# Kernel optimization log

Hardware: AMD Instinct MI355X
Metric: run time of the kernel (lower is better)

## Reference

```python
import jax, jax.numpy as jnp
from jax import lax
import numpy as np

BATCH, SEQ, VOCAB, EMB, UNIT = 256, 512, 50000, 128, 512


def setup_inputs() -> dict:
    key = jax.random.key(0)
    ks = jax.random.split(key, 8)
    s = 0.05  # keep tanh out of saturation
    return {
        "tokens": jax.random.randint(ks[0], (BATCH, SEQ), 0, VOCAB, dtype=jnp.int32),
        "emb": jax.random.normal(ks[1], (VOCAB, EMB), jnp.float32) * s,
        "Wx0": jax.random.normal(ks[2], (EMB, UNIT), jnp.float32) * s,
        "Wh0": jax.random.normal(ks[3], (UNIT, UNIT), jnp.float32) * s,
        "b0": jnp.zeros((UNIT,), jnp.float32),
        "Wx1": jax.random.normal(ks[4], (UNIT, UNIT), jnp.float32) * s,
        "Wh1": jax.random.normal(ks[5], (UNIT, UNIT), jnp.float32) * s,
        "b1": jnp.zeros((UNIT,), jnp.float32),
        "fc_w": jax.random.normal(ks[6], (UNIT, 1), jnp.float32) * s,
        "fc_b": jnp.zeros((1,), jnp.float32),
    }


def reference(tokens, emb, Wx0, Wh0, b0, Wx1, Wh1, b1, fc_w, fc_b):
    # Embedding lookup: [B, T, E]
    x = emb[tokens]
    B = tokens.shape[0]
    U = Wh0.shape[0]

    def step(carry, xt):
        h0, h1, h2 = carry
        # SimpleRNNCell: h' = tanh(x @ Wx + h @ Wh + b); dropout inactive (training=None)
        h0n = jnp.tanh(xt @ Wx0 + h0 @ Wh0 + b0)
        # NOTE: original code reuses rnncell1 weights for both layer 1 and layer 2 (bug kept)
        h1n = jnp.tanh(h0n @ Wx1 + h1 @ Wh1 + b1)
        h2n = jnp.tanh(h1n @ Wx1 + h2 @ Wh1 + b1)
        return (h0n, h1n, h2n), None

    init = tuple(jnp.zeros((B, U), x.dtype) for _ in range(3))
    (h0, h1, h2), _ = lax.scan(step, init, jnp.swapaxes(x, 0, 1))  # scan over time [T, B, E]
    logits = h2 @ fc_w + fc_b  # [B, 1]
    return jax.nn.sigmoid(logits)
```

## Files before the change

### kernel.cpp

```cpp
#include <hip/hip_runtime.h>


#define BATCH 256
#define SEQ   512
#define EMBD  128
#define UNIT  512

typedef _Float16 half8 __attribute__((ext_vector_type(8)));
typedef _Float16 half4 __attribute__((ext_vector_type(4)));
typedef float    f32x4 __attribute__((ext_vector_type(4)));
typedef unsigned int uint4v __attribute__((ext_vector_type(4)));
typedef int      int4v __attribute__((ext_vector_type(4)));

#define FLAGS_BYTES 4096
#define HBUF_OFF    4096
#define HBUF_ELEMS  (3*8*4*32*512)
#define HBUF_BYTES  (HBUF_ELEMS*2)
#define PWX0_OFF    (HBUF_OFF + HBUF_BYTES)
#define PWH0_OFF    (PWX0_OFF + EMBD*UNIT*2)
#define PWX1_OFF    (PWH0_OFF + UNIT*UNIT*2)
#define PWH1_OFF    (PWX1_OFF + UNIT*UNIT*2)

__device__ __forceinline__ void sc_st_int(int* p, int v) {
    asm volatile("global_store_dword %0, %1, off sc0 sc1" :: "v"(p), "v"(v) : "memory");
}

__device__ __forceinline__ void sc_ld_q3(const int* p0, const int* p1, const int* p2,
                                         int4v& a, int4v& b, int4v& c) {
    asm volatile(
        "global_load_dwordx4 %0, %3, off sc0 sc1\n\t"
        "global_load_dwordx4 %1, %4, off sc0 sc1\n\t"
        "global_load_dwordx4 %2, %5, off sc0 sc1\n\t"
        "s_waitcnt vmcnt(0)"
        : "=&v"(a), "=&v"(b), "=&v"(c)
        : "v"(p0), "v"(p1), "v"(p2)
        : "memory");
}

__device__ __forceinline__ void sc_load14(
    const uint4v* a0, const uint4v* a1, const uint4v* a2,
    const uint4v* a3, const uint4v* a4, const uint4v* a5,
    const uint4v* b0, const uint4v* b1, const uint4v* b2, const uint4v* b3,
    const uint4v* b4, const uint4v* b5, const uint4v* b6, const uint4v* b7,
    uint4v& s0, uint4v& s1, uint4v& s2, uint4v& s3, uint4v& s4, uint4v& s5,
    uint4v& r0, uint4v& r1, uint4v& r2, uint4v& r3,
    uint4v& r4, uint4v& r5, uint4v& r6, uint4v& r7)
{
    asm volatile(
        "global_load_dwordx4 %0, %14, off sc0 sc1\n\t"
        "global_load_dwordx4 %1, %15, off sc0 sc1\n\t"
        "global_load_dwordx4 %2, %16, off sc0 sc1\n\t"
        "global_load_dwordx4 %3, %17, off sc0 sc1\n\t"
        "global_load_dwordx4 %4, %18, off sc0 sc1\n\t"
        "global_load_dwordx4 %5, %19, off sc0 sc1\n\t"
        "global_load_dwordx4 %6, %20, off sc0 sc1\n\t"
        "global_load_dwordx4 %7, %21, off sc0 sc1\n\t"
        "global_load_dwordx4 %8, %22, off sc0 sc1\n\t"
        "global_load_dwordx4 %9, %23, off sc0 sc1\n\t"
        "global_load_dwordx4 %10, %24, off sc0 sc1\n\t"
        "global_load_dwordx4 %11, %25, off sc0 sc1\n\t"
        "global_load_dwordx4 %12, %26, off sc0 sc1\n\t"
        "global_load_dwordx4 %13, %27, off sc0 sc1\n\t"
        "s_waitcnt vmcnt(0)"
        : "=&v"(s0), "=&v"(s1), "=&v"(s2), "=&v"(s3), "=&v"(s4), "=&v"(s5),
          "=&v"(r0), "=&v"(r1), "=&v"(r2), "=&v"(r3),
          "=&v"(r4), "=&v"(r5), "=&v"(r6), "=&v"(r7)
        : "v"(a0), "v"(a1), "v"(a2), "v"(a3), "v"(a4), "v"(a5),
          "v"(b0), "v"(b1), "v"(b2), "v"(b3), "v"(b4), "v"(b5), "v"(b6), "v"(b7)
        : "memory");
}

__device__ __forceinline__ void sc_load6(
    const uint4v* p0, const uint4v* p1, const uint4v* p2,
    const uint4v* p3, const uint4v* p4, const uint4v* p5,
    uint4v& r0, uint4v& r1, uint4v& r2, uint4v& r3, uint4v& r4, uint4v& r5)
{
    asm volatile(
        "global_load_dwordx4 %0, %6, off sc0 sc1\n\t"
        "global_load_dwordx4 %1, %7, off sc0 sc1\n\t"
        "global_load_dwordx4 %2, %8, off sc0 sc1\n\t"
        "global_load_dwordx4 %3, %9, off sc0 sc1\n\t"
        "global_load_dwordx4 %4, %10, off sc0 sc1\n\t"
        "global_load_dwordx4 %5, %11, off sc0 sc1\n\t"
        "s_waitcnt vmcnt(0)"
        : "=&v"(r0), "=&v"(r1), "=&v"(r2), "=&v"(r3), "=&v"(r4), "=&v"(r5)
        : "v"(p0), "v"(p1), "v"(p2), "v"(p3), "v"(p4), "v"(p5)
        : "memory");
}

__device__ __forceinline__ void sc_store2(uint4v* p0, uint4v v0, uint4v* p1, uint4v v1) {
    asm volatile(
        "global_store_dwordx4 %0, %2, off sc0 sc1\n\t"
        "global_store_dwordx4 %1, %3, off sc0 sc1\n\t"
        "s_waitcnt vmcnt(0)"
        :: "v"(p0), "v"(p1), "v"(v0), "v"(v1)
        : "memory");
}

__global__ void zero_ws_kernel(uint4v* __restrict__ p, int n16) {
    int i = blockIdx.x * 256 + threadIdx.x;
    uint4v z = {0u, 0u, 0u, 0u};
    if (i < n16) p[i] = z;
}

__global__ void pack_w_kernel(const float* __restrict__ src, _Float16* __restrict__ dst,
                              int K, int N) {
    int idx = blockIdx.x * 256 + threadIdx.x;
    if (idx >= K * N) return;
    int j    = idx & 7;
    int lane = (idx >> 3) & 63;
    int rest = idx >> 9;
    int KT   = K >> 5;
    int kt   = rest % KT;
    int nt   = rest / KT;
    int k = kt*32 + (lane >> 4)*8 + j;
    int n = nt*16 + (lane & 15);
    dst[idx] = (_Float16)src[k * N + n];
}

__global__ __launch_bounds__(256, 1)
void rnn_main_kernel(const int*   __restrict__ tokens,
                     const float* __restrict__ emb,
                     const float* __restrict__ b0,
                     const float* __restrict__ b1,
                     char* ws)
{
    const int bid   = blockIdx.x;
    const int layer = bid >> 5;
    const int mg    = (bid >> 2) & 7;
    const int ns    = bid & 3;
    const int tid   = threadIdx.x;
    const int wv    = tid >> 6;
    const int lane  = tid & 63;
    const int q     = lane >> 4;
    const int c16   = lane & 15;

    int* flags = (int*)ws;
    int* qOwn  = flags + (layer*8 + mg)*32;
    int* qUp   = flags + ((layer > 0 ? layer-1 : layer)*8 + mg)*32;
    int* qDn   = flags + ((layer < 2 ? layer+1 : layer)*8 + mg)*32;

    _Float16* hbuf = (_Float16*)(ws + HBUF_OFF);
    const _Float16* pWh = (const _Float16*)(ws + (layer == 0 ? PWH0_OFF : PWH1_OFF));
    const _Float16* pWx = (const _Float16*)(ws + (layer == 0 ? PWX0_OFF : PWX1_OFF));
    const float* bias = (layer == 0) ? b0 : b1;

    const int c0  = ns*128 + wv*32;
    const int nt0 = c0 >> 4;

    __shared__ _Float16 Ah [32][512];
    __shared__ _Float16 Ain[32][512];
    __shared__ _Float16 Bounce[32][128];

    {
        uint4v z = {0u,0u,0u,0u};
#pragma unroll
        for (int i = 0; i < 8; ++i) ((uint4v*)Ah)[i*256 + tid] = z;
    }

    half8 whf[16][2];
    half8 wxf[16][2];
#pragma unroll
    for (int kt = 0; kt < 16; ++kt)
#pragma unroll
        for (int n = 0; n < 2; ++n)
            whf[kt][n] = *(const half8*)&pWh[(((nt0 + n)*16 + kt)*64 + lane) * 8];
    if (layer == 0) {
#pragma unroll
        for (int kt = 0; kt < 4; ++kt)
#pragma unroll
            for (int n = 0; n < 2; ++n)
                wxf[kt][n] = *(const half8*)&pWx[(((nt0 + n)*4 + kt)*64 + lane) * 8];
    } else {
#pragma unroll
        for (int kt = 0; kt < 16; ++kt)
#pragma unroll
            for (int n = 0; n < 2; ++n)
                wxf[kt][n] = *(const half8*)&pWx[(((nt0 + n)*16 + kt)*64 + lane) * 8];
    }

    const float bv0 = bias[c0 + c16];
    const float bv1 = bias[c0 + 16 + c16];

    const int m0       = mg * 32;
    const int slotBase = (layer*8 + mg) * 4;

    const int sA = (ns == 0) ? 1 : 0;
    const int sB = (ns <= 1) ? 2 : 1;
    const int sC = (ns <= 2) ? 3 : 2;

    for (int t = 0; t < SEQ; ++t) {
        if (tid == 0) {
            for (;;) {
                int4v o, u, d;
                sc_ld_q3(qOwn, qUp, qDn, o, u, d);
                int mo = o[0] < o[1] ? o[0] : o[1];
                mo = mo < o[2] ? mo : o[2]; mo = mo < o[3] ? mo : o[3];
                int mu = u[0] < u[1] ? u[0] : u[1];
                mu = mu < u[2] ? mu : u[2]; mu = mu < u[3] ? mu : u[3];
                int md = d[0] < d[1] ? d[0] : d[1];
                md = md < d[2] ? md : d[2]; md = md < d[3] ? md : d[3];
                bool ok = (mo >= t);
                if (layer > 0)            ok = ok && (mu >= t + 1);
                if (layer < 2 && t >= 4)  ok = ok && (md >= t - 3);
                if (ok) break;
                __builtin_amdgcn_s_sleep(1);
            }
        }
        __syncthreads();

        const uint4v* tp = (const uint4v*)(hbuf + (slotBase + ((t + 3) & 3)) * 16384);
        const int j0 = 2*tid, j1 = j0 + 1;
        const int r0i = j0 >> 4, cl0 = j0 & 15;
        const int r1i = j1 >> 4, cl1 = j1 & 15;
        const int ccA0 = sA*16 + cl0, ccA1 = sA*16 + cl1;
        const int ccB0 = sB*16 + cl0, ccB1 = sB*16 + cl1;
        const int ccC0 = sC*16 + cl0, ccC1 = sC*16 + cl1;

        f32x4 acc00 = {0,0,0,0}, acc01 = {0,0,0,0}, acc10 = {0,0,0,0}, acc11 = {0,0,0,0};

        if (layer > 0) {
            const uint4v* sb = (const uint4v*)
                (hbuf + (((layer-1)*8 + mg)*4 + (t & 3)) * 16384);
            uint4v s0,s1,s2,s3,s4,s5, rr0,rr1,rr2,rr3,rr4,rr5,rr6,rr7;
            sc_load14(tp + r0i*64 + ccA0, tp + r1i*64 + ccA1,
                      tp + r0i*64 + ccB0, tp + r1i*64 + ccB1,
                      tp + r0i*64 + ccC0, tp + r1i*64 + ccC1,
                      sb +        tid, sb +  256 + tid, sb +  512 + tid, sb +  768 + tid,
                      sb + 1024 + tid, sb + 1280 + tid, sb + 1536 + tid, sb + 1792 + tid,
                      s0, s1, s2, s3, s4, s5,
                      rr0, rr1, rr2, rr3, rr4, rr5, rr6, rr7);
            *(uint4v*)&Ah[r0i][((ccA0 + r0i) & 63) * 8] = s0;
            *(uint4v*)&Ah[r1i][((ccA1 + r1i) & 63) * 8] = s1;
            *(uint4v*)&Ah[r0i][((ccB0 + r0i) & 63) * 8] = s2;
            *(uint4v*)&Ah[r1i][((ccB1 + r1i) & 63) * 8] = s3;
            *(uint4v*)&Ah[r0i][((ccC0 + r0i) & 63) * 8] = s4;
            *(uint4v*)&Ah[r1i][((ccC1 + r1i) & 63) * 8] = s5;
#pragma unroll
            for (int i = 0; i < 8; ++i) {
                uint4v v = (i==0)?rr0:(i==1)?rr1:(i==2)?rr2:(i==3)?rr3:
                           (i==4)?rr4:(i==5)?rr5:(i==6)?rr6:rr7;
                int ci = i*256 + tid;
                int r  = ci >> 6;
                int cc = ci & 63;
                *(uint4v*)&Ain[r][((cc + r) & 63) * 8] = v;
            }
            __syncthreads();

#pragma unroll
            for (int kt = 0; kt < 16; ++kt) {
                half8 a0 = *(const half8*)&Ah[c16]     [((kt*4 + q + c16)      & 63) * 8];
                half8 a1 = *(const half8*)&Ah[16 + c16][((kt*4 + q + 16 + c16) & 63) * 8];
                acc00 = __builtin_amdgcn_mfma_f32_16x16x32_f16(a0, whf[kt][0], acc00, 0, 0, 0);
                acc01 = __builtin_amdgcn_mfma_f32_16x16x32_f16(a0, whf[kt][1], acc01, 0, 0, 0);
                acc10 = __builtin_amdgcn_mfma_f32_16x16x32_f16(a1, whf[kt][0], acc10, 0, 0, 0);
                acc11 = __builtin_amdgcn_mfma_f32_16x16x32_f16(a1, whf[kt][1], acc11, 0, 0, 0);
            }
#pragma unroll
            for (int kt = 0; kt < 16; ++kt) {
                half8 a0 = *(const half8*)&Ain[c16]     [((kt*4 + q + c16)      & 63) * 8];
                half8 a1 = *(const half8*)&Ain[16 + c16][((kt*4 + q + 16 + c16) & 63) * 8];
                acc00 = __builtin_amdgcn_mfma_f32_16x16x32_f16(a0, wxf[kt][0], acc00, 0, 0, 0);
                acc01 = __builtin_amdgcn_mfma_f32_16x16x32_f16(a0, wxf[kt][1], acc01, 0, 0, 0);
                acc10 = __builtin_amdgcn_mfma_f32_16x16x32_f16(a1, wxf[kt][0], acc10, 0, 0, 0);
                acc11 = __builtin_amdgcn_mfma_f32_16x16x32_f16(a1, wxf[kt][1], acc11, 0, 0, 0);
            }
        } else {
            uint4v s0, s1, s2, s3, s4, s5;
            sc_load6(tp + r0i*64 + ccA0, tp + r1i*64 + ccA1,
                     tp + r0i*64 + ccB0, tp + r1i*64 + ccB1,
                     tp + r0i*64 + ccC0, tp + r1i*64 + ccC1,
                     s0, s1, s2, s3, s4, s5);
            *(uint4v*)&Ah[r0i][((ccA0 + r0i) & 63) * 8] = s0;
            *(uint4v*)&Ah[r1i][((ccA1 + r1i) & 63) * 8] = s1;
            *(uint4v*)&Ah[r0i][((ccB0 + r0i) & 63) * 8] = s2;
            *(uint4v*)&Ah[r1i][((ccB1 + r1i) & 63) * 8] = s3;
            *(uint4v*)&Ah[r0i][((ccC0 + r0i) & 63) * 8] = s4;
            *(uint4v*)&Ah[r1i][((ccC1 + r1i) & 63) * 8] = s5;
#pragma unroll
            for (int i = 0; i < 4; ++i) {
                int idx = i*256 + tid;
                int r   = idx >> 5;
                int qq  = idx & 31;
                int tok = tokens[(m0 + r)*SEQ + t];
                float4 f = *((const float4*)(emb + (long)tok * EMBD) + qq);
                half4 h = { (_Float16)f.x, (_Float16)f.y, (_Float16)f.z, (_Float16)f.w };
                *(half4*)&Ain[r][((((qq >> 1) + r) & 63) * 8) + (qq & 1) * 4] = h;
            }
            __syncthreads();

#pragma unroll
            for (int kt = 0; kt < 16; ++kt) {
                half8 a0 = *(const half8*)&Ah[c16]     [((kt*4 + q + c16)      & 63) * 8];
                half8 a1 = *(const half8*)&Ah[16 + c16][((kt*4 + q + 16 + c16) & 63) * 8];
                acc00 = __builtin_amdgcn_mfma_f32_16x16x32_f16(a0, whf[kt][0], acc00, 0, 0, 0);
                acc01 = __builtin_amdgcn_mfma_f32_16x16x32_f16(a0, whf[kt][1], acc01, 0, 0, 0);
                acc10 = __builtin_amdgcn_mfma_f32_16x16x32_f16(a1, whf[kt][0], acc10, 0, 0, 0);
                acc11 = __builtin_amdgcn_mfma_f32_16x16x32_f16(a1, whf[kt][1], acc11, 0, 0, 0);
            }
#pragma unroll
            for (int kt = 0; kt < 4; ++kt) {
                half8 a0 = *(const half8*)&Ain[c16]     [((kt*4 + q + c16)      & 63) * 8];
                half8 a1 = *(const half8*)&Ain[16 + c16][((kt*4 + q + 16 + c16) & 63) * 8];
                acc00 = __builtin_amdgcn_mfma_f32_16x16x32_f16(a0, wxf[kt][0], acc00, 0, 0, 0);
                acc01 = __builtin_amdgcn_mfma_f32_16x16x32_f16(a0, wxf[kt][1], acc01, 0, 0, 0);
                acc10 = __builtin_amdgcn_mfma_f32_16x16x32_f16(a1, wxf[kt][0], acc10, 0, 0, 0);
                acc11 = __builtin_amdgcn_mfma_f32_16x16x32_f16(a1, wxf[kt][1], acc11, 0, 0, 0);
            }
        }

        _Float16 hv[16];
#pragma unroll
        for (int r = 0; r < 4; ++r) {
            int row0 = q*4 + r, row1 = 16 + row0;
            float z, e; _Float16 v;
            z = acc00[r] + bv0; e = __expf(2.0f*z); v = (_Float16)(1.0f - 2.0f/(e + 1.0f));
            hv[r*4+0] = v; Bounce[row0][wv*32 + c16]      = v;
            z = acc01[r] + bv1; e = __expf(2.0f*z); v = (_Float16)(1.0f - 2.0f/(e + 1.0f));
            hv[r*4+1] = v; Bounce[row0][wv*32 + 16 + c16] = v;
            z = acc10[r] + bv0; e = __expf(2.0f*z); v = (_Float16)(1.0f - 2.0f/(e + 1.0f));
            hv[r*4+2] = v; Bounce[row1][wv*32 + c16]      = v;
            z = acc11[r] + bv1; e = __expf(2.0f*z); v = (_Float16)(1.0f - 2.0f/(e + 1.0f));
            hv[r*4+3] = v; Bounce[row1][wv*32 + 16 + c16] = v;
        }
        __syncthreads();

        {
            int g0 = c0 + c16, g1 = c0 + 16 + c16;
#pragma unroll
            for (int r = 0; r < 4; ++r) {
                int row0 = q*4 + r, row1 = 16 + row0;
                Ah[row0][(((g0 >> 3) + row0) & 63)*8 + (g0 & 7)] = hv[r*4+0];
                Ah[row0][(((g1 >> 3) + row0) & 63)*8 + (g1 & 7)] = hv[r*4+1];
                Ah[row1][(((g0 >> 3) + row1) & 63)*8 + (g0 & 7)] = hv[r*4+2];
                Ah[row1][(((g1 >> 3) + row1) & 63)*8 + (g1 & 7)] = hv[r*4+3];
            }
            _Float16* tc = hbuf + (slotBase + (t & 3)) * 16384;
            uint4v v0 = ((const uint4v*)Bounce)[j0];
            uint4v v1 = ((const uint4v*)Bounce)[j1];
            uint4v* d0 = (uint4v*)(tc + (j0 >> 4)*512 + ns*128) + (j0 & 15);
            uint4v* d1 = (uint4v*)(tc + (j1 >> 4)*512 + ns*128) + (j1 & 15);
            sc_store2(d0, v0, d1, v1);
        }
        __syncthreads();
        if (tid == 0) sc_st_int(qOwn + ns, t + 1);
    }
}

__global__ void fc_kernel(const char* __restrict__ ws,
                          const float* __restrict__ fc_w,
                          const float* __restrict__ fc_b,
                          float* __restrict__ out)
{
    int row  = blockIdx.x;
    int lane = threadIdx.x;
    int m = row >> 5, lr = row & 31;
    const _Float16* h2 = (const _Float16*)(ws + HBUF_OFF)
                         + (((2*8 + m)*4 + 3) * 16384)
                         + lr * UNIT;
    half8 hv = *(const half8*)&h2[lane * 8];
    const float* w = fc_w + lane * 8;
    float s = 0.0f;
#pragma unroll
    for (int j = 0; j < 8; ++j) s += (float)hv[j] * w[j];
#pragma unroll
    for (int off = 32; off > 0; off >>= 1) s += __shfl_down(s, off);
    if (lane == 0) {
        float logit = s + fc_b[0];
        out[row] = 1.0f / (1.0f + __expf(-logit));
    }
}

extern "C" void kernel_launch(void* const* d_in, const int* in_sizes, int n_in,
                              void* d_out, int out_size, void* d_ws, size_t ws_size,
                              hipStream_t stream)
{
    const int*   tokens = (const int*)  d_in[0];
    const float* emb    = (const float*)d_in[1];
    const float* Wx0    = (const float*)d_in[2];
    const float* Wh0    = (const float*)d_in[3];
    const float* b0     = (const float*)d_in[4];
    const float* Wx1    = (const float*)d_in[5];
    const float* Wh1    = (const float*)d_in[6];
    const float* b1     = (const float*)d_in[7];
    const float* fcw    = (const float*)d_in[8];
    const float* fcb    = (const float*)d_in[9];
    char*  ws  = (char*)d_ws;
    float* out = (float*)d_out;

    int n16 = (FLAGS_BYTES + HBUF_BYTES) / 16;
    zero_ws_kernel<<<(n16 + 255)/256, 256, 0, stream>>>((uint4v*)ws, n16);

    pack_w_kernel<<<(EMBD*UNIT + 255)/256, 256, 0, stream>>>(Wx0, (_Float16*)(ws + PWX0_OFF), EMBD, UNIT);
    pack_w_kernel<<<(UNIT*UNIT + 255)/256, 256, 0, stream>>>(Wh0, (_Float16*)(ws + PWH0_OFF), UNIT, UNIT);
    pack_w_kernel<<<(UNIT*UNIT + 255)/256, 256, 0, stream>>>(Wx1, (_Float16*)(ws + PWX1_OFF), UNIT, UNIT);
    pack_w_kernel<<<(UNIT*UNIT + 255)/256, 256, 0, stream>>>(Wh1, (_Float16*)(ws + PWH1_OFF), UNIT, UNIT);

    rnn_main_kernel<<<96, 256, 0, stream>>>(tokens, emb, b0, b1, ws);

    fc_kernel<<<256, 64, 0, stream>>>((const char*)ws, fcw, fcb, out);
}
```

Baseline: 2.632 ms.

## Piggyback flag reads on data loads to skip spin-wait and prefetch embeddings

The peer-progress flags are now loaded in the same batched coherent load as the hidden-state data. Their minimum is cached in shared memory, so the per-step spin-wait and its barrier can be skipped when earlier reads already show the dependencies are met. Layer 0 also prefetches the next step's embedding rows into registers during the current step and writes them to LDS after the MMA work. This hides the gather latency but adds registers and some extra flag loads.

```diff
diff --git a/kernel.cpp b/kernel.cpp
--- a/kernel.cpp
+++ b/kernel.cpp
@@ -23,6 +23,12 @@
 
 __device__ __forceinline__ void sc_st_int(int* p, int v) {
     asm volatile("global_store_dword %0, %1, off sc0 sc1" :: "v"(p), "v"(v) : "memory");
+}
+
+__device__ __forceinline__ int min4(int4v v) {
+    int a = v[0] < v[1] ? v[0] : v[1];
+    int b = v[2] < v[3] ? v[2] : v[3];
+    return a < b ? a : b;
 }
 
 __device__ __forceinline__ void sc_ld_q3(const int* p0, const int* p1, const int* p2,
@@ -37,54 +43,68 @@
         : "memory");
 }
 
-__device__ __forceinline__ void sc_load14(
+__device__ __forceinline__ void sc_load17(
     const uint4v* a0, const uint4v* a1, const uint4v* a2,
     const uint4v* a3, const uint4v* a4, const uint4v* a5,
     const uint4v* b0, const uint4v* b1, const uint4v* b2, const uint4v* b3,
     const uint4v* b4, const uint4v* b5, const uint4v* b6, const uint4v* b7,
+    const int* f0, const int* f1, const int* f2,
     uint4v& s0, uint4v& s1, uint4v& s2, uint4v& s3, uint4v& s4, uint4v& s5,
     uint4v& r0, uint4v& r1, uint4v& r2, uint4v& r3,
-    uint4v& r4, uint4v& r5, uint4v& r6, uint4v& r7)
+    uint4v& r4, uint4v& r5, uint4v& r6, uint4v& r7,
+    int4v& q0, int4v& q1, int4v& q2)
 {
     asm volatile(
-        "global_load_dwordx4 %0, %14, off sc0 sc1\n\t"
-        "global_load_dwordx4 %1, %15, off sc0 sc1\n\t"
-        "global_load_dwordx4 %2, %16, off sc0 sc1\n\t"
-        "global_load_dwordx4 %3, %17, off sc0 sc1\n\t"
-        "global_load_dwordx4 %4, %18, off sc0 sc1\n\t"
-        "global_load_dwordx4 %5, %19, off sc0 sc1\n\t"
-        "global_load_dwordx4 %6, %20, off sc0 sc1\n\t"
-        "global_load_dwordx4 %7, %21, off sc0 sc1\n\t"
-        "global_load_dwordx4 %8, %22, off sc0 sc1\n\t"
-        "global_load_dwordx4 %9, %23, off sc0 sc1\n\t"
-        "global_load_dwordx4 %10, %24, off sc0 sc1\n\t"
-        "global_load_dwordx4 %11, %25, off sc0 sc1\n\t"
-        "global_load_dwordx4 %12, %26, off sc0 sc1\n\t"
-        "global_load_dwordx4 %13, %27, off sc0 sc1\n\t"
+        "global_load_dwordx4 %0, %17, off sc0 sc1\n\t"
+        "global_load_dwordx4 %1, %18, off sc0 sc1\n\t"
+        "global_load_dwordx4 %2, %19, off sc0 sc1\n\t"
+        "global_load_dwordx4 %3, %20, off sc0 sc1\n\t"
+        "global_load_dwordx4 %4, %21, off sc0 sc1\n\t"
+        "global_load_dwordx4 %5, %22, off sc0 sc1\n\t"
+        "global_load_dwordx4 %6, %23, off sc0 sc1\n\t"
+        "global_load_dwordx4 %7, %24, off sc0 sc1\n\t"
+        "global_load_dwordx4 %8, %25, off sc0 sc1\n\t"
+        "global_load_dwordx4 %9, %26, off sc0 sc1\n\t"
+        "global_load_dwordx4 %10, %27, off sc0 sc1\n\t"
+        "global_load_dwordx4 %11, %28, off sc0 sc1\n\t"
+        "global_load_dwordx4 %12, %29, off sc0 sc1\n\t"
+        "global_load_dwordx4 %13, %30, off sc0 sc1\n\t"
+        "global_load_dwordx4 %14, %31, off sc0 sc1\n\t"
+        "global_load_dwordx4 %15, %32, off sc0 sc1\n\t"
+        "global_load_dwordx4 %16, %33, off sc0 sc1\n\t"
         "s_waitcnt vmcnt(0)"
         : "=&v"(s0), "=&v"(s1), "=&v"(s2), "=&v"(s3), "=&v"(s4), "=&v"(s5),
           "=&v"(r0), "=&v"(r1), "=&v"(r2), "=&v"(r3),
-          "=&v"(r4), "=&v"(r5), "=&v"(r6), "=&v"(r7)
+          "=&v"(r4), "=&v"(r5), "=&v"(r6), "=&v"(r7),
+          "=&v"(q0), "=&v"(q1), "=&v"(q2)
         : "v"(a0), "v"(a1), "v"(a2), "v"(a3), "v"(a4), "v"(a5),
-          "v"(b0), "v"(b1), "v"(b2), "v"(b3), "v"(b4), "v"(b5), "v"(b6), "v"(b7)
+          "v"(b0), "v"(b1), "v"(b2), "v"(b3), "v"(b4), "v"(b5), "v"(b6), "v"(b7),
+          "v"(f0), "v"(f1), "v"(f2)
         : "memory");
 }
 
-__device__ __forceinline__ void sc_load6(
+__device__ __forceinline__ void sc_load9(
     const uint4v* p0, const uint4v* p1, const uint4v* p2,
     const uint4v* p3, const uint4v* p4, const uint4v* p5,
-    uint4v& r0, uint4v& r1, uint4v& r2, uint4v& r3, uint4v& r4, uint4v& r5)
+    const int* f0, const int* f1, const int* f2,
+    uint4v& r0, uint4v& r1, uint4v& r2, uint4v& r3, uint4v& r4, uint4v& r5,
+    int4v& q0, int4v& q1, int4v& q2)
 {
     asm volatile(
-        "global_load_dwordx4 %0, %6, off sc0 sc1\n\t"
-        "global_load_dwordx4 %1, %7, off sc0 sc1\n\t"
-        "global_load_dwordx4 %2, %8, off sc0 sc1\n\t"
-        "global_load_dwordx4 %3, %9, off sc0 sc1\n\t"
-        "global_load_dwordx4 %4, %10, off sc0 sc1\n\t"
-        "global_load_dwordx4 %5, %11, off sc0 sc1\n\t"
+        "global_load_dwordx4 %0, %9, off sc0 sc1\n\t"
+        "global_load_dwordx4 %1, %10, off sc0 sc1\n\t"
+        "global_load_dwordx4 %2, %11, off sc0 sc1\n\t"
+        "global_load_dwordx4 %3, %12, off sc0 sc1\n\t"
+        "global_load_dwordx4 %4, %13, off sc0 sc1\n\t"
+        "global_load_dwordx4 %5, %14, off sc0 sc1\n\t"
+        "global_load_dwordx4 %6, %15, off sc0 sc1\n\t"
+        "global_load_dwordx4 %7, %16, off sc0 sc1\n\t"
+        "global_load_dwordx4 %8, %17, off sc0 sc1\n\t"
         "s_waitcnt vmcnt(0)"
-        : "=&v"(r0), "=&v"(r1), "=&v"(r2), "=&v"(r3), "=&v"(r4), "=&v"(r5)
-        : "v"(p0), "v"(p1), "v"(p2), "v"(p3), "v"(p4), "v"(p5)
+        : "=&v"(r0), "=&v"(r1), "=&v"(r2), "=&v"(r3), "=&v"(r4), "=&v"(r5),
+          "=&v"(q0), "=&v"(q1), "=&v"(q2)
+        : "v"(p0), "v"(p1), "v"(p2), "v"(p3), "v"(p4), "v"(p5),
+          "v"(f0), "v"(f1), "v"(f2)
         : "memory");
 }
 
@@ -151,12 +171,14 @@
     __shared__ _Float16 Ah [32][512];
     __shared__ _Float16 Ain[32][512];
     __shared__ _Float16 Bounce[32][128];
+    __shared__ int      SkipInfo[4];
 
     {
         uint4v z = {0u,0u,0u,0u};
 #pragma unroll
         for (int i = 0; i < 8; ++i) ((uint4v*)Ah)[i*256 + tid] = z;
     }
+    if (tid < 4) SkipInfo[tid] = -1000000;
 
     half8 whf[16][2];
     half8 wxf[16][2];
@@ -189,25 +211,42 @@
     const int sB = (ns <= 1) ? 2 : 1;
     const int sC = (ns <= 2) ? 3 : 2;
 
+    if (layer == 0) {
+#pragma unroll
+        for (int i = 0; i < 4; ++i) {
+            int idx = i*256 + tid;
+            int r   = idx >> 5;
+            int qq  = idx & 31;
+            int tok = tokens[(m0 + r)*SEQ + 0];
+            float4 f = *((const float4*)(emb + (long)tok * EMBD) + qq);
+            half4 h = { (_Float16)f.x, (_Float16)f.y, (_Float16)f.z, (_Float16)f.w };
+            *(half4*)&Ain[r][((((qq >> 1) + r) & 63) * 8) + (qq & 1) * 4] = h;
+        }
+    }
+    __syncthreads();
+
     for (int t = 0; t < SEQ; ++t) {
-        if (tid == 0) {
-            for (;;) {
-                int4v o, u, d;
-                sc_ld_q3(qOwn, qUp, qDn, o, u, d);
-                int mo = o[0] < o[1] ? o[0] : o[1];
-                mo = mo < o[2] ? mo : o[2]; mo = mo < o[3] ? mo : o[3];
-                int mu = u[0] < u[1] ? u[0] : u[1];
-                mu = mu < u[2] ? mu : u[2]; mu = mu < u[3] ? mu : u[3];
-                int md = d[0] < d[1] ? d[0] : d[1];
-                md = md < d[2] ? md : d[2]; md = md < d[3] ? md : d[3];
-                bool ok = (mo >= t);
-                if (layer > 0)            ok = ok && (mu >= t + 1);
-                if (layer < 2 && t >= 4)  ok = ok && (md >= t - 3);
-                if (ok) break;
-                __builtin_amdgcn_s_sleep(1);
+        {
+            int mo = SkipInfo[0], mu = SkipInfo[1], md = SkipInfo[2];
+            bool skip = (mo >= t);
+            if (layer > 0)           skip = skip && (mu >= t + 1);
+            if (layer < 2 && t >= 4) skip = skip && (md >= t - 3);
+            if (!skip) {
+                if (tid == 0) {
+                    for (;;) {
+                        int4v o, u, d;
+                        sc_ld_q3(qOwn, qUp, qDn, o, u, d);
+                        int o_ = min4(o), u_ = min4(u), d_ = min4(d);
+                        bool ok = (o_ >= t);
+                        if (layer > 0)            ok = ok && (u_ >= t + 1);
+                        if (layer < 2 && t >= 4)  ok = ok && (d_ >= t - 3);
+                        if (ok) { SkipInfo[0]=o_; SkipInfo[1]=u_; SkipInfo[2]=d_; break; }
+                        __builtin_amdgcn_s_sleep(2);
+                    }
+                }
+                __syncthreads();
             }
         }
-        __syncthreads();
 
         const uint4v* tp = (const uint4v*)(hbuf + (slotBase + ((t + 3) & 3)) * 16384);
         const int j0 = 2*tid, j1 = j0 + 1;
@@ -218,18 +257,22 @@
         const int ccC0 = sC*16 + cl0, ccC1 = sC*16 + cl1;
 
         f32x4 acc00 = {0,0,0,0}, acc01 = {0,0,0,0}, acc10 = {0,0,0,0}, acc11 = {0,0,0,0};
+        int4v fq0, fq1, fq2;
+        float4 pg0, pg1, pg2, pg3;
 
         if (layer > 0) {
             const uint4v* sb = (const uint4v*)
                 (hbuf + (((layer-1)*8 + mg)*4 + (t & 3)) * 16384);
             uint4v s0,s1,s2,s3,s4,s5, rr0,rr1,rr2,rr3,rr4,rr5,rr6,rr7;
-            sc_load14(tp + r0i*64 + ccA0, tp + r1i*64 + ccA1,
+            sc_load17(tp + r0i*64 + ccA0, tp + r1i*64 + ccA1,
                       tp + r0i*64 + ccB0, tp + r1i*64 + ccB1,
                       tp + r0i*64 + ccC0, tp + r1i*64 + ccC1,
                       sb +        tid, sb +  256 + tid, sb +  512 + tid, sb +  768 + tid,
                       sb + 1024 + tid, sb + 1280 + tid, sb + 1536 + tid, sb + 1792 + tid,
+                      qOwn, qUp, qDn,
                       s0, s1, s2, s3, s4, s5,
-                      rr0, rr1, rr2, rr3, rr4, rr5, rr6, rr7);
+                      rr0, rr1, rr2, rr3, rr4, rr5, rr6, rr7,
+                      fq0, fq1, fq2);
             *(uint4v*)&Ah[r0i][((ccA0 + r0i) & 63) * 8] = s0;
             *(uint4v*)&Ah[r1i][((ccA1 + r1i) & 63) * 8] = s1;
             *(uint4v*)&Ah[r0i][((ccB0 + r0i) & 63) * 8] = s2;
@@ -267,25 +310,32 @@
             }
         } else {
             uint4v s0, s1, s2, s3, s4, s5;
-            sc_load6(tp + r0i*64 + ccA0, tp + r1i*64 + ccA1,
+            sc_load9(tp + r0i*64 + ccA0, tp + r1i*64 + ccA1,
                      tp + r0i*64 + ccB0, tp + r1i*64 + ccB1,
                      tp + r0i*64 + ccC0, tp + r1i*64 + ccC1,
-                     s0, s1, s2, s3, s4, s5);
+                     qOwn, qUp, qDn,
+                     s0, s1, s2, s3, s4, s5, fq0, fq1, fq2);
             *(uint4v*)&Ah[r0i][((ccA0 + r0i) & 63) * 8] = s0;
             *(uint4v*)&Ah[r1i][((ccA1 + r1i) & 63) * 8] = s1;
             *(uint4v*)&Ah[r0i][((ccB0 + r0i) & 63) * 8] = s2;
             *(uint4v*)&Ah[r1i][((ccB1 + r1i) & 63) * 8] = s3;
             *(uint4v*)&Ah[r0i][((ccC0 + r0i) & 63) * 8] = s4;
             *(uint4v*)&Ah[r1i][((ccC1 + r1i) & 63) * 8] = s5;
-#pragma unroll
-            for (int i = 0; i < 4; ++i) {
-                int idx = i*256 + tid;
-                int r   = idx >> 5;
-                int qq  = idx & 31;
-                int tok = tokens[(m0 + r)*SEQ + t];
-                float4 f = *((const float4*)(emb + (long)tok * EMBD) + qq);
-                half4 h = { (_Float16)f.x, (_Float16)f.y, (_Float16)f.z, (_Float16)f.w };
-                *(half4*)&Ain[r][((((qq >> 1) + r) & 63) * 8) + (qq & 1) * 4] = h;
+
+            {
+                int tn = (t + 1 < SEQ) ? t + 1 : SEQ - 1;
+                int idx0 = tid,        r0g = idx0 >> 5, q0g = idx0 & 31;
+                int idx1 = 256 + tid,  r1g = idx1 >> 5, q1g = idx1 & 31;
+                int idx2 = 512 + tid,  r2g = idx2 >> 5, q2g = idx2 & 31;
+                int idx3 = 768 + tid,  r3g = idx3 >> 5, q3g = idx3 & 31;
+                int t0 = tokens[(m0 + r0g)*SEQ + tn];
+                int t1 = tokens[(m0 + r1g)*SEQ + tn];
+                int t2 = tokens[(m0 + r2g)*SEQ + tn];
+                int t3 = tokens[(m0 + r3g)*SEQ + tn];
+                pg0 = *((const float4*)(emb + (long)t0 * EMBD) + q0g);
+                pg1 = *((const float4*)(emb + (long)t1 * EMBD) + q1g);
+                pg2 = *((const float4*)(emb + (long)t2 * EMBD) + q2g);
+                pg3 = *((const float4*)(emb + (long)t3 * EMBD) + q3g);
             }
             __syncthreads();
 
@@ -334,6 +384,22 @@
                 Ah[row0][(((g1 >> 3) + row0) & 63)*8 + (g1 & 7)] = hv[r*4+1];
                 Ah[row1][(((g0 >> 3) + row1) & 63)*8 + (g0 & 7)] = hv[r*4+2];
                 Ah[row1][(((g1 >> 3) + row1) & 63)*8 + (g1 & 7)] = hv[r*4+3];
+            }
+            if (layer == 0 && t + 1 < SEQ) {
+#pragma unroll
+                for (int i = 0; i < 4; ++i) {
+                    float4 f = (i==0)?pg0:(i==1)?pg1:(i==2)?pg2:pg3;
+                    int idx = i*256 + tid;
+                    int r   = idx >> 5;
+                    int qq  = idx & 31;
+                    half4 h = { (_Float16)f.x, (_Float16)f.y, (_Float16)f.z, (_Float16)f.w };
+                    *(half4*)&Ain[r][((((qq >> 1) + r) & 63) * 8) + (qq & 1) * 4] = h;
+                }
+            }
+            if (tid == 0) {
+                SkipInfo[0] = min4(fq0);
+                SkipInfo[1] = min4(fq1);
+                SkipInfo[2] = min4(fq2);
             }
             _Float16* tc = hbuf + (slotBase + (t & 3)) * 16384;
             uint4v v0 = ((const uint4v*)Bounce)[j0];
```

New measurement: 2.755 ms. 4.7% more time.

## Overlap input loads with recurrent MFMA via LDS DMA, prefetch, and XOR swizzle

Applied to the files above, without the earlier changes.

Layers 1 and 2 now pull the previous layer's hidden state straight into LDS with global_load_lds DMA. That DMA runs while the Wh MFMA loop executes, so the Wx loop waits only on its own barrier. Layer 0 prefetches the next step's embedding rows into registers during the current step and writes them to LDS after the tanh. The LDS layout changes from a rotate swizzle to an XOR swizzle, and the global h buffer is stored in the same swizzled order so the copy needs no per-element reshuffle; fc_kernel is adjusted to match. The code also replaces __syncthreads with lighter waitcnt+barrier sequences and adds a per-block staggered startup sleep, at the cost of more complex memory ordering that depends on the asm waitcnt choices being correct.

```diff
diff --git a/kernel.cpp b/kernel.cpp
--- a/kernel.cpp
+++ b/kernel.cpp
@@ -34,39 +34,6 @@
         "s_waitcnt vmcnt(0)"
         : "=&v"(a), "=&v"(b), "=&v"(c)
         : "v"(p0), "v"(p1), "v"(p2)
-        : "memory");
-}
-
-__device__ __forceinline__ void sc_load14(
-    const uint4v* a0, const uint4v* a1, const uint4v* a2,
-    const uint4v* a3, const uint4v* a4, const uint4v* a5,
-    const uint4v* b0, const uint4v* b1, const uint4v* b2, const uint4v* b3,
-    const uint4v* b4, const uint4v* b5, const uint4v* b6, const uint4v* b7,
-    uint4v& s0, uint4v& s1, uint4v& s2, uint4v& s3, uint4v& s4, uint4v& s5,
-    uint4v& r0, uint4v& r1, uint4v& r2, uint4v& r3,
-    uint4v& r4, uint4v& r5, uint4v& r6, uint4v& r7)
-{
-    asm volatile(
-        "global_load_dwordx4 %0, %14, off sc0 sc1\n\t"
-        "global_load_dwordx4 %1, %15, off sc0 sc1\n\t"
-        "global_load_dwordx4 %2, %16, off sc0 sc1\n\t"
-        "global_load_dwordx4 %3, %17, off sc0 sc1\n\t"
-        "global_load_dwordx4 %4, %18, off sc0 sc1\n\t"
-        "global_load_dwordx4 %5, %19, off sc0 sc1\n\t"
-        "global_load_dwordx4 %6, %20, off sc0 sc1\n\t"
-        "global_load_dwordx4 %7, %21, off sc0 sc1\n\t"
-        "global_load_dwordx4 %8, %22, off sc0 sc1\n\t"
-        "global_load_dwordx4 %9, %23, off sc0 sc1\n\t"
-        "global_load_dwordx4 %10, %24, off sc0 sc1\n\t"
-        "global_load_dwordx4 %11, %25, off sc0 sc1\n\t"
-        "global_load_dwordx4 %12, %26, off sc0 sc1\n\t"
-        "global_load_dwordx4 %13, %27, off sc0 sc1\n\t"
-        "s_waitcnt vmcnt(0)"
-        : "=&v"(s0), "=&v"(s1), "=&v"(s2), "=&v"(s3), "=&v"(s4), "=&v"(s5),
-          "=&v"(r0), "=&v"(r1), "=&v"(r2), "=&v"(r3),
-          "=&v"(r4), "=&v"(r5), "=&v"(r6), "=&v"(r7)
-        : "v"(a0), "v"(a1), "v"(a2), "v"(a3), "v"(a4), "v"(a5),
-          "v"(b0), "v"(b1), "v"(b2), "v"(b3), "v"(b4), "v"(b5), "v"(b6), "v"(b7)
         : "memory");
 }
 
@@ -97,6 +64,23 @@
         : "memory");
 }
 
+__device__ __forceinline__ void bar_lgkm() {
+    asm volatile("s_waitcnt lgkmcnt(0)\n\ts_barrier" ::: "memory");
+}
+__device__ __forceinline__ void bar_vm_lgkm() {
+    asm volatile("s_waitcnt vmcnt(0) lgkmcnt(0)\n\ts_barrier" ::: "memory");
+}
+__device__ __forceinline__ void bar_only() {
+    asm volatile("s_barrier" ::: "memory");
+}
+
+__device__ __forceinline__ void lds_dma16(const void* g, void* l) {
+    __builtin_amdgcn_global_load_lds(
+        (const __attribute__((address_space(1))) void*)g,
+        (__attribute__((address_space(3))) void*)l,
+        16, 0, 17);
+}
+
 __global__ void zero_ws_kernel(uint4v* __restrict__ p, int n16) {
     int i = blockIdx.x * 256 + threadIdx.x;
     uint4v z = {0u, 0u, 0u, 0u};
@@ -134,6 +118,9 @@
     const int lane  = tid & 63;
     const int q     = lane >> 4;
     const int c16   = lane & 15;
+    const int xq    = c16 & 7;
+
+    for (int i = 0; i < mg; ++i) { __builtin_amdgcn_s_sleep(8); __builtin_amdgcn_s_sleep(8); }
 
     int* flags = (int*)ws;
     int* qOwn  = flags + (layer*8 + mg)*32;
@@ -188,6 +175,31 @@
     const int sA = (ns == 0) ? 1 : 0;
     const int sB = (ns <= 1) ? 2 : 1;
     const int sC = (ns <= 2) ? 3 : 2;
+
+    const int j0 = 2*tid, j1 = j0 + 1;
+    const int r0i = j0 >> 4, cl0 = j0 & 15;
+    const int r1i = j1 >> 4, cl1 = j1 & 15;
+    const int k0 = r0i & 7, k1 = r1i & 7;
+    const int pA0 = sA*16 + cl0, pA1 = sA*16 + cl1;
+    const int pB0 = sB*16 + cl0, pB1 = sB*16 + cl1;
+    const int pC0 = sC*16 + cl0, pC1 = sC*16 + cl1;
+    const int pO0 = (ns*16 + cl0) ^ k0;
+    const int pO1 = (ns*16 + cl1) ^ k1;
+
+    if (layer == 0) {
+#pragma unroll
+        for (int i = 0; i < 4; ++i) {
+            int idx = i*256 + tid;
+            int r   = idx >> 5;
+            int qq  = idx & 31;
+            int tok = tokens[(m0 + r)*SEQ + 0];
+            float4 f = *((const float4*)(emb + (long)tok * EMBD) + qq);
+            half4 h = { (_Float16)f.x, (_Float16)f.y, (_Float16)f.z, (_Float16)f.w };
+            int pc = (qq >> 1) ^ (r & 7);
+            *(half4*)&Ain[r][pc*8 + (qq & 1)*4] = h;
+        }
+    }
+    __syncthreads();
 
     for (int t = 0; t < SEQ; ++t) {
         if (tid == 0) {
@@ -207,101 +219,78 @@
                 __builtin_amdgcn_s_sleep(1);
             }
         }
-        __syncthreads();
+        bar_only();
 
         const uint4v* tp = (const uint4v*)(hbuf + (slotBase + ((t + 3) & 3)) * 16384);
-        const int j0 = 2*tid, j1 = j0 + 1;
-        const int r0i = j0 >> 4, cl0 = j0 & 15;
-        const int r1i = j1 >> 4, cl1 = j1 & 15;
-        const int ccA0 = sA*16 + cl0, ccA1 = sA*16 + cl1;
-        const int ccB0 = sB*16 + cl0, ccB1 = sB*16 + cl1;
-        const int ccC0 = sC*16 + cl0, ccC1 = sC*16 + cl1;
+
+        {
+            uint4v s0, s1, s2, s3, s4, s5;
+            sc_load6(tp + r0i*64 + pA0, tp + r1i*64 + pA1,
+                     tp + r0i*64 + pB0, tp + r1i*64 + pB1,
+                     tp + r0i*64 + pC0, tp + r1i*64 + pC1,
+                     s0, s1, s2, s3, s4, s5);
+            *(uint4v*)&Ah[r0i][pA0 * 8] = s0;
+            *(uint4v*)&Ah[r1i][pA1 * 8] = s1;
+            *(uint4v*)&Ah[r0i][pB0 * 8] = s2;
+            *(uint4v*)&Ah[r1i][pB1 * 8] = s3;
+            *(uint4v*)&Ah[r0i][pC0 * 8] = s4;
+            *(uint4v*)&Ah[r1i][pC1 * 8] = s5;
+        }
+
+        float4 pg0, pg1, pg2, pg3;
+        if (layer > 0) {
+            const _Float16* sb = hbuf + (((layer-1)*8 + mg)*4 + (t & 3)) * 16384;
+#pragma unroll
+            for (int i = 0; i < 8; ++i) {
+                int row = wv*8 + i;
+                lds_dma16(sb + row*512 + lane*8, &Ain[row][0]);
+            }
+        } else {
+            int tn = (t + 1 < SEQ) ? t + 1 : SEQ - 1;
+            int idx0 = tid,        r0g = idx0 >> 5, q0g = idx0 & 31;
+            int idx1 = 256 + tid,  r1g = idx1 >> 5, q1g = idx1 & 31;
+            int idx2 = 512 + tid,  r2g = idx2 >> 5, q2g = idx2 & 31;
+            int idx3 = 768 + tid,  r3g = idx3 >> 5, q3g = idx3 & 31;
+            int t0 = tokens[(m0 + r0g)*SEQ + tn];
+            int t1 = tokens[(m0 + r1g)*SEQ + tn];
+            int t2 = tokens[(m0 + r2g)*SEQ + tn];
+            int t3 = tokens[(m0 + r3g)*SEQ + tn];
+            pg0 = *((const float4*)(emb + (long)t0 * EMBD) + q0g);
+            pg1 = *((const float4*)(emb + (long)t1 * EMBD) + q1g);
+            pg2 = *((const float4*)(emb + (long)t2 * EMBD) + q2g);
+            pg3 = *((const float4*)(emb + (long)t3 * EMBD) + q3g);
+        }
+
+        bar_lgkm();
 
         f32x4 acc00 = {0,0,0,0}, acc01 = {0,0,0,0}, acc10 = {0,0,0,0}, acc11 = {0,0,0,0};
 
+#pragma unroll
+        for (int kt = 0; kt < 16; ++kt) {
+            half8 a0 = *(const half8*)&Ah[c16]     [((kt*4 + q) ^ xq) * 8];
+            half8 a1 = *(const half8*)&Ah[16 + c16][((kt*4 + q) ^ xq) * 8];
+            acc00 = __builtin_amdgcn_mfma_f32_16x16x32_f16(a0, whf[kt][0], acc00, 0, 0, 0);
+            acc01 = __builtin_amdgcn_mfma_f32_16x16x32_f16(a0, whf[kt][1], acc01, 0, 0, 0);
+            acc10 = __builtin_amdgcn_mfma_f32_16x16x32_f16(a1, whf[kt][0], acc10, 0, 0, 0);
+            acc11 = __builtin_amdgcn_mfma_f32_16x16x32_f16(a1, whf[kt][1], acc11, 0, 0, 0);
+        }
+
         if (layer > 0) {
-            const uint4v* sb = (const uint4v*)
-                (hbuf + (((layer-1)*8 + mg)*4 + (t & 3)) * 16384);
-            uint4v s0,s1,s2,s3,s4,s5, rr0,rr1,rr2,rr3,rr4,rr5,rr6,rr7;
-            sc_load14(tp + r0i*64 + ccA0, tp + r1i*64 + ccA1,
-                      tp + r0i*64 + ccB0, tp + r1i*64 + ccB1,
-                      tp + r0i*64 + ccC0, tp + r1i*64 + ccC1,
-                      sb +        tid, sb +  256 + tid, sb +  512 + tid, sb +  768 + tid,
-                      sb + 1024 + tid, sb + 1280 + tid, sb + 1536 + tid, sb + 1792 + tid,
-                      s0, s1, s2, s3, s4, s5,
-                      rr0, rr1, rr2, rr3, rr4, rr5, rr6, rr7);
-            *(uint4v*)&Ah[r0i][((ccA0 + r0i) & 63) * 8] = s0;
-            *(uint4v*)&Ah[r1i][((ccA1 + r1i) & 63) * 8] = s1;
-            *(uint4v*)&Ah[r0i][((ccB0 + r0i) & 63) * 8] = s2;
-            *(uint4v*)&Ah[r1i][((ccB1 + r1i) & 63) * 8] = s3;
-            *(uint4v*)&Ah[r0i][((ccC0 + r0i) & 63) * 8] = s4;
-            *(uint4v*)&Ah[r1i][((ccC1 + r1i) & 63) * 8] = s5;
-#pragma unroll
-            for (int i = 0; i < 8; ++i) {
-                uint4v v = (i==0)?rr0:(i==1)?rr1:(i==2)?rr2:(i==3)?rr3:
-                           (i==4)?rr4:(i==5)?rr5:(i==6)?rr6:rr7;
-                int ci = i*256 + tid;
-                int r  = ci >> 6;
-                int cc = ci & 63;
-                *(uint4v*)&Ain[r][((cc + r) & 63) * 8] = v;
-            }
-            __syncthreads();
-
+            bar_vm_lgkm();
 #pragma unroll
             for (int kt = 0; kt < 16; ++kt) {
-                half8 a0 = *(const half8*)&Ah[c16]     [((kt*4 + q + c16)      & 63) * 8];
-                half8 a1 = *(const half8*)&Ah[16 + c16][((kt*4 + q + 16 + c16) & 63) * 8];
-                acc00 = __builtin_amdgcn_mfma_f32_16x16x32_f16(a0, whf[kt][0], acc00, 0, 0, 0);
-                acc01 = __builtin_amdgcn_mfma_f32_16x16x32_f16(a0, whf[kt][1], acc01, 0, 0, 0);
-                acc10 = __builtin_amdgcn_mfma_f32_16x16x32_f16(a1, whf[kt][0], acc10, 0, 0, 0);
-                acc11 = __builtin_amdgcn_mfma_f32_16x16x32_f16(a1, whf[kt][1], acc11, 0, 0, 0);
-            }
-#pragma unroll
-            for (int kt = 0; kt < 16; ++kt) {
-                half8 a0 = *(const half8*)&Ain[c16]     [((kt*4 + q + c16)      & 63) * 8];
-                half8 a1 = *(const half8*)&Ain[16 + c16][((kt*4 + q + 16 + c16) & 63) * 8];
+                half8 a0 = *(const half8*)&Ain[c16]     [((kt*4 + q) ^ xq) * 8];
+                half8 a1 = *(const half8*)&Ain[16 + c16][((kt*4 + q) ^ xq) * 8];
                 acc00 = __builtin_amdgcn_mfma_f32_16x16x32_f16(a0, wxf[kt][0], acc00, 0, 0, 0);
                 acc01 = __builtin_amdgcn_mfma_f32_16x16x32_f16(a0, wxf[kt][1], acc01, 0, 0, 0);
                 acc10 = __builtin_amdgcn_mfma_f32_16x16x32_f16(a1, wxf[kt][0], acc10, 0, 0, 0);
                 acc11 = __builtin_amdgcn_mfma_f32_16x16x32_f16(a1, wxf[kt][1], acc11, 0, 0, 0);
             }
         } else {
-            uint4v s0, s1, s2, s3, s4, s5;
-            sc_load6(tp + r0i*64 + ccA0, tp + r1i*64 + ccA1,
-                     tp + r0i*64 + ccB0, tp + r1i*64 + ccB1,
-                     tp + r0i*64 + ccC0, tp + r1i*64 + ccC1,
-                     s0, s1, s2, s3, s4, s5);
-            *(uint4v*)&Ah[r0i][((ccA0 + r0i) & 63) * 8] = s0;
-            *(uint4v*)&Ah[r1i][((ccA1 + r1i) & 63) * 8] = s1;
-            *(uint4v*)&Ah[r0i][((ccB0 + r0i) & 63) * 8] = s2;
-            *(uint4v*)&Ah[r1i][((ccB1 + r1i) & 63) * 8] = s3;
-            *(uint4v*)&Ah[r0i][((ccC0 + r0i) & 63) * 8] = s4;
-            *(uint4v*)&Ah[r1i][((ccC1 + r1i) & 63) * 8] = s5;
-#pragma unroll
-            for (int i = 0; i < 4; ++i) {
-                int idx = i*256 + tid;
-                int r   = idx >> 5;
-                int qq  = idx & 31;
-                int tok = tokens[(m0 + r)*SEQ + t];
-                float4 f = *((const float4*)(emb + (long)tok * EMBD) + qq);
-                half4 h = { (_Float16)f.x, (_Float16)f.y, (_Float16)f.z, (_Float16)f.w };
-                *(half4*)&Ain[r][((((qq >> 1) + r) & 63) * 8) + (qq & 1) * 4] = h;
-            }
-            __syncthreads();
-
-#pragma unroll
-            for (int kt = 0; kt < 16; ++kt) {
-                half8 a0 = *(const half8*)&Ah[c16]     [((kt*4 + q + c16)      & 63) * 8];
-                half8 a1 = *(const half8*)&Ah[16 + c16][((kt*4 + q + 16 + c16) & 63) * 8];
-                acc00 = __builtin_amdgcn_mfma_f32_16x16x32_f16(a0, whf[kt][0], acc00, 0, 0, 0);
-                acc01 = __builtin_amdgcn_mfma_f32_16x16x32_f16(a0, whf[kt][1], acc01, 0, 0, 0);
-                acc10 = __builtin_amdgcn_mfma_f32_16x16x32_f16(a1, whf[kt][0], acc10, 0, 0, 0);
-                acc11 = __builtin_amdgcn_mfma_f32_16x16x32_f16(a1, whf[kt][1], acc11, 0, 0, 0);
-            }
 #pragma unroll
             for (int kt = 0; kt < 4; ++kt) {
-                half8 a0 = *(const half8*)&Ain[c16]     [((kt*4 + q + c16)      & 63) * 8];
-                half8 a1 = *(const half8*)&Ain[16 + c16][((kt*4 + q + 16 + c16) & 63) * 8];
+                half8 a0 = *(const half8*)&Ain[c16]     [((kt*4 + q) ^ xq) * 8];
+                half8 a1 = *(const half8*)&Ain[16 + c16][((kt*4 + q) ^ xq) * 8];
                 acc00 = __builtin_amdgcn_mfma_f32_16x16x32_f16(a0, wxf[kt][0], acc00, 0, 0, 0);
                 acc01 = __builtin_amdgcn_mfma_f32_16x16x32_f16(a0, wxf[kt][1], acc01, 0, 0, 0);
                 acc10 = __builtin_amdgcn_mfma_f32_16x16x32_f16(a1, wxf[kt][0], acc10, 0, 0, 0);
@@ -309,40 +298,43 @@
             }
         }
 
-        _Float16 hv[16];
 #pragma unroll
         for (int r = 0; r < 4; ++r) {
             int row0 = q*4 + r, row1 = 16 + row0;
-            float z, e; _Float16 v;
-            z = acc00[r] + bv0; e = __expf(2.0f*z); v = (_Float16)(1.0f - 2.0f/(e + 1.0f));
-            hv[r*4+0] = v; Bounce[row0][wv*32 + c16]      = v;
-            z = acc01[r] + bv1; e = __expf(2.0f*z); v = (_Float16)(1.0f - 2.0f/(e + 1.0f));
-            hv[r*4+1] = v; Bounce[row0][wv*32 + 16 + c16] = v;
-            z = acc10[r] + bv0; e = __expf(2.0f*z); v = (_Float16)(1.0f - 2.0f/(e + 1.0f));
-            hv[r*4+2] = v; Bounce[row1][wv*32 + c16]      = v;
-            z = acc11[r] + bv1; e = __expf(2.0f*z); v = (_Float16)(1.0f - 2.0f/(e + 1.0f));
-            hv[r*4+3] = v; Bounce[row1][wv*32 + 16 + c16] = v;
-        }
-        __syncthreads();
+            float z, e;
+            z = acc00[r] + bv0; e = __expf(2.0f*z);
+            Bounce[row0][wv*32 + c16]      = (_Float16)(1.0f - 2.0f/(e + 1.0f));
+            z = acc01[r] + bv1; e = __expf(2.0f*z);
+            Bounce[row0][wv*32 + 16 + c16] = (_Float16)(1.0f - 2.0f/(e + 1.0f));
+            z = acc10[r] + bv0; e = __expf(2.0f*z);
+            Bounce[row1][wv*32 + c16]      = (_Float16)(1.0f - 2.0f/(e + 1.0f));
+            z = acc11[r] + bv1; e = __expf(2.0f*z);
+            Bounce[row1][wv*32 + 16 + c16] = (_Float16)(1.0f - 2.0f/(e + 1.0f));
+        }
+        bar_lgkm();
 
         {
-            int g0 = c0 + c16, g1 = c0 + 16 + c16;
-#pragma unroll
-            for (int r = 0; r < 4; ++r) {
-                int row0 = q*4 + r, row1 = 16 + row0;
-                Ah[row0][(((g0 >> 3) + row0) & 63)*8 + (g0 & 7)] = hv[r*4+0];
-                Ah[row0][(((g1 >> 3) + row0) & 63)*8 + (g1 & 7)] = hv[r*4+1];
-                Ah[row1][(((g0 >> 3) + row1) & 63)*8 + (g0 & 7)] = hv[r*4+2];
-                Ah[row1][(((g1 >> 3) + row1) & 63)*8 + (g1 & 7)] = hv[r*4+3];
+            uint4v v0 = *(const uint4v*)&Bounce[r0i][cl0 * 8];
+            uint4v v1 = *(const uint4v*)&Bounce[r1i][cl1 * 8];
+            *(uint4v*)&Ah[r0i][pO0 * 8] = v0;
+            *(uint4v*)&Ah[r1i][pO1 * 8] = v1;
+            if (layer == 0 && t + 1 < SEQ) {
+#pragma unroll
+                for (int i = 0; i < 4; ++i) {
+                    float4 f = (i==0)?pg0:(i==1)?pg1:(i==2)?pg2:pg3;
+                    int idx = i*256 + tid;
+                    int r   = idx >> 5;
+                    int qq  = idx & 31;
+                    half4 h = { (_Float16)f.x, (_Float16)f.y, (_Float16)f.z, (_Float16)f.w };
+                    int pc = (qq >> 1) ^ (r & 7);
+                    *(half4*)&Ain[r][pc*8 + (qq & 1)*4] = h;
+                }
             }
             _Float16* tc = hbuf + (slotBase + (t & 3)) * 16384;
-            uint4v v0 = ((const uint4v*)Bounce)[j0];
-            uint4v v1 = ((const uint4v*)Bounce)[j1];
-            uint4v* d0 = (uint4v*)(tc + (j0 >> 4)*512 + ns*128) + (j0 & 15);
-            uint4v* d1 = (uint4v*)(tc + (j1 >> 4)*512 + ns*128) + (j1 & 15);
-            sc_store2(d0, v0, d1, v1);
-        }
-        __syncthreads();
+            sc_store2((uint4v*)(tc + r0i*512) + pO0, v0,
+                      (uint4v*)(tc + r1i*512) + pO1, v1);
+        }
+        bar_lgkm();
         if (tid == 0) sc_st_int(qOwn + ns, t + 1);
     }
 }
@@ -359,7 +351,8 @@
                          + (((2*8 + m)*4 + 3) * 16384)
                          + lr * UNIT;
     half8 hv = *(const half8*)&h2[lane * 8];
-    const float* w = fc_w + lane * 8;
+    int c = lane ^ (lr & 7);
+    const float* w = fc_w + c * 8;
     float s = 0.0f;
 #pragma unroll
     for (int j = 0; j < 8; ++j) s += (float)hv[j] * w[j];
```

Result: slower. 2.919 ms (+10.9%).
